# Kernel tuning notes

Measured on AMD Instinct MI355X. Metric: run time of the kernel, lower is better.

The kernel has to match this reference:

```python
import jax, jax.numpy as jnp
import numpy as np

N_NODES = 50000
N_EDGES = 800000
N_GRAPHS = 256
IN_CH = 128
HID = 256
FFN = 256
OUT = 1


def xavier(key, shape):
    fan_in, fan_out = shape[0], shape[1]
    a = jnp.sqrt(6.0 / (fan_in + fan_out))
    return jax.random.uniform(key, shape, jnp.float32, -a, a)


def setup_inputs() -> dict:
    key = jax.random.key(0)
    ks = jax.random.split(key, 12)
    x = jax.random.normal(ks[0], (N_NODES, IN_CH), jnp.float32)
    edge_index = jax.random.randint(ks[1], (2, N_EDGES), 0, N_NODES, jnp.int32)
    batch = jnp.sort(jax.random.randint(ks[2], (N_NODES,), 0, N_GRAPHS, jnp.int32))
    return {
        "x": x,
        "edge_index": edge_index,
        "batch": batch,
        # GCNConv layers (glorot weight, zero bias as in PyG reset_parameters)
        "W1": xavier(ks[3], (IN_CH, HID)), "b1": jnp.zeros((HID,), jnp.float32),
        "W2": xavier(ks[4], (HID, HID)),   "b2": jnp.zeros((HID,), jnp.float32),
        "W3": xavier(ks[5], (HID, HID)),   "b3": jnp.zeros((HID,), jnp.float32),
        # FFN: Linear(HID, FFN) then final Linear(FFN, OUT)
        "Wf": xavier(ks[6], (HID, FFN)),   "bf": jnp.zeros((FFN,), jnp.float32),
        "Wo": xavier(ks[7], (FFN, OUT)),   "bo": jnp.zeros((OUT,), jnp.float32),
    }


def _gcn_norm(edge_index, n_nodes):
    # add self-loops, compute symmetric normalization D^-1/2 (A+I) D^-1/2
    loops = jnp.arange(n_nodes, dtype=edge_index.dtype)
    row = jnp.concatenate([edge_index[0], loops])
    col = jnp.concatenate([edge_index[1], loops])
    deg = jax.ops.segment_sum(jnp.ones_like(col, jnp.float32), col, num_segments=n_nodes)
    dis = jnp.where(deg > 0, jax.lax.rsqrt(jnp.maximum(deg, 1.0)), 0.0)
    norm = dis[row] * dis[col]  # [E+N]
    return row, col, norm


def _gcn_conv(x, W, b, row, col, norm, n_nodes):
    xw = x @ W                                   # [N, H]
    msg = xw[row] * norm[:, None]                # gather + scale  [E+N, H]
    out = jax.ops.segment_sum(msg, col, num_segments=n_nodes)
    return out + b


def reference(x, edge_index, batch, W1, b1, W2, b2, W3, b3, Wf, bf, Wo, bo):
    row, col, norm = _gcn_norm(edge_index, N_NODES)
    h = jax.nn.relu(_gcn_conv(x, W1, b1, row, col, norm, N_NODES))
    h = jax.nn.relu(_gcn_conv(h, W2, b2, row, col, norm, N_NODES))
    h = jax.nn.relu(_gcn_conv(h, W3, b3, row, col, norm, N_NODES))
    # global mean pool over graphs
    counts = jax.ops.segment_sum(jnp.ones((N_NODES,), jnp.float32), batch, num_segments=N_GRAPHS)
    pooled = jax.ops.segment_sum(h, batch, num_segments=N_GRAPHS) / jnp.maximum(counts, 1.0)[:, None]
    # FFN (dropout is identity in eval mode): Linear -> ReLU -> final Linear
    g = jax.nn.relu(pooled @ Wf + bf)
    out = g @ Wo + bo
    return out
```

## Files before the change

### kernel.cpp

```cpp
#include <hip/hip_runtime.h>
#include <hip/hip_bf16.h>
#include <hip/hip_fp16.h>


#define THREADS 256

typedef _Float16 f16x8 __attribute__((ext_vector_type(8)));
typedef float    f32x4 __attribute__((ext_vector_type(4)));
typedef unsigned short u16x8 __attribute__((ext_vector_type(8)));


__global__ void degree_goff_kernel(const int* __restrict__ col, int* __restrict__ deg, int E,
                                   const int* __restrict__ batch, int* __restrict__ goff,
                                   int N, int G) {
    int i = blockIdx.x * THREADS + threadIdx.x;
    if (i < E) atomicAdd(&deg[col[i]], 1);
    if (i < N) {
        int b1 = batch[i];
        int b0 = (i == 0) ? -1 : batch[i - 1];
        for (int g = b0 + 1; g <= b1; ++g) goff[g] = i;
        if (i == N - 1) {
            for (int g = b1 + 1; g <= G; ++g) goff[g] = N;
        }
    }
}

__global__ __launch_bounds__(256) void scanA_kernel(
    const int* __restrict__ in, int* __restrict__ out, int* __restrict__ bsum,
    float* __restrict__ dis, int n) {
    __shared__ int wsum[4];
    int i0 = blockIdx.x * 1024 + threadIdx.x * 4;
    int lane = threadIdx.x & 63, wid = threadIdx.x >> 6;
    int v0 = 0, v1 = 0, v2 = 0, v3 = 0;
    if (i0 + 3 < n) {
        int4 v = *(const int4*)&in[i0];
        v0 = v.x; v1 = v.y; v2 = v.z; v3 = v.w;
    } else {
        if (i0 + 0 < n) v0 = in[i0 + 0];
        if (i0 + 1 < n) v1 = in[i0 + 1];
        if (i0 + 2 < n) v2 = in[i0 + 2];
        if (i0 + 3 < n) v3 = in[i0 + 3];
    }
    if (i0 + 0 < n) dis[i0 + 0] = rsqrtf((float)(v0 + 1));
    if (i0 + 1 < n) dis[i0 + 1] = rsqrtf((float)(v1 + 1));
    if (i0 + 2 < n) dis[i0 + 2] = rsqrtf((float)(v2 + 1));
    if (i0 + 3 < n) dis[i0 + 3] = rsqrtf((float)(v3 + 1));
    v0 = (v0 + 7) & ~7; v1 = (v1 + 7) & ~7;
    v2 = (v2 + 7) & ~7; v3 = (v3 + 7) & ~7;
    int s = v0 + v1 + v2 + v3;
    int inc = s;
    #pragma unroll
    for (int d = 1; d < 64; d <<= 1) {
        int t = __shfl_up(inc, d);
        if (lane >= d) inc += t;
    }
    if (lane == 63) wsum[wid] = inc;
    __syncthreads();
    int add = 0;
    for (int w = 0; w < wid; ++w) add += wsum[w];
    int ex = add + inc - s;
    if (i0 + 0 < n) out[i0 + 0] = ex;
    if (i0 + 1 < n) out[i0 + 1] = ex + v0;
    if (i0 + 2 < n) out[i0 + 2] = ex + v0 + v1;
    if (i0 + 3 < n) out[i0 + 3] = ex + v0 + v1 + v2;
    if (threadIdx.x == 255) bsum[blockIdx.x] = add + inc;
}

__global__ void scanB_kernel(int* __restrict__ bsum, int* __restrict__ total_slot, int nb) {
    int lane = threadIdx.x;
    int v = (lane < nb) ? bsum[lane] : 0;
    int inc = v;
    #pragma unroll
    for (int d = 1; d < 64; d <<= 1) {
        int t = __shfl_up(inc, d);
        if (lane >= d) inc += t;
    }
    if (lane < nb) bsum[lane] = inc - v;
    if (lane == 63) *total_slot = inc;
}

__global__ void padfill_kernel(const int* __restrict__ offs, const int* __restrict__ deg,
                               unsigned short* __restrict__ srcs, int N) {
    int c = blockIdx.x * THREADS + threadIdx.x;
    if (c < N) {
        int s = offs[c] + deg[c], e = offs[c + 1];
        for (int i = s; i < e; ++i) srcs[i] = (unsigned short)N;
    }
}

__global__ void csr_fill_kernel(const int* __restrict__ row, const int* __restrict__ col,
                                const int* __restrict__ offs, int* __restrict__ deg,
                                unsigned short* __restrict__ srcs, int E) {
    int e = blockIdx.x * THREADS + threadIdx.x;
    if (e < E) {
        int c = col[e];
        int old = atomicSub(&deg[c], 1);
        srcs[offs[c] + old - 1] = (unsigned short)row[e];
    }
}

__global__ void convert_kernel(
    int* __restrict__ offs, const int* __restrict__ bsum, int Nfix,
    const float* __restrict__ X, const float* __restrict__ dis,
    _Float16* __restrict__ Xs, int total8, int IC,
    const float* __restrict__ W1, _Float16* __restrict__ W1t, int k1,
    const float* __restrict__ W2, _Float16* __restrict__ W2t,
    const float* __restrict__ W3, _Float16* __restrict__ W3t,
    _Float16* __restrict__ Hs) {
    int i = blockIdx.x * THREADS + threadIdx.x;
    if (i < Nfix) {
        offs[i] += bsum[i >> 10];
        return;
    }
    int j = i - Nfix;
    int Ms = Nfix + 1;
    if (j < total8) {
        int idx = j * 8;
        int node = idx / IC;
        int ch0  = idx % IC;
        float d = dis[node];
        float4 a = *(const float4*)&X[idx];
        float4 b = *(const float4*)&X[idx + 4];
        f16x8 o;
        o[0] = (_Float16)(d * a.x); o[1] = (_Float16)(d * a.y);
        o[2] = (_Float16)(d * a.z); o[3] = (_Float16)(d * a.w);
        o[4] = (_Float16)(d * b.x); o[5] = (_Float16)(d * b.y);
        o[6] = (_Float16)(d * b.z); o[7] = (_Float16)(d * b.w);
        int sw = IC >> 3;
        int slice = ch0 / sw, within = ch0 % sw;
        *(f16x8*)&Xs[((size_t)slice * Ms + node) * sw + within] = o;
        return;
    }
    j -= total8;
    int n1 = k1 * 256;
    if (j < n1) {
        int k = j >> 8, n = j & 255;
        W1t[n * k1 + k] = (_Float16)W1[j];
        return;
    }
    j -= n1;
    if (j < 65536) {
        int k = j >> 8, n = j & 255;
        W2t[n * 256 + k] = (_Float16)W2[j];
        return;
    }
    j -= 65536;
    if (j < 65536) {
        int k = j >> 8, n = j & 255;
        W3t[n * 256 + k] = (_Float16)W3[j];
        return;
    }
    j -= 65536;
    {
        int swx = IC >> 3;
        int nx = 8 * swx;
        if (j < nx) {
            int slice = j / swx, wi = j % swx;
            Xs[((size_t)slice * Ms + Nfix) * swx + wi] = (_Float16)0.f;
            return;
        }
        j -= nx;
        if (j < 256) {
            int slice = j >> 5, wi = j & 31;
            Hs[((size_t)slice * Ms + Nfix) * 32 + wi] = (_Float16)0.f;
        }
    }
}


template<int CH>
__global__ __launch_bounds__(256) void aggregate_slice_kernel(
    const _Float16* __restrict__ X, const int* __restrict__ offs,
    const unsigned short* __restrict__ srcs, const float* __restrict__ dis,
    _Float16* __restrict__ A, int N) {
    constexpr int LPN = CH / 64;
    constexpr int NPB = 256 / LPN;
    int bid   = blockIdx.x;
    int slice = bid & 7;
    int tile  = bid >> 3;
    int node  = tile * NPB + threadIdx.x / LPN;
    if (node >= N) return;
    int lane = threadIdx.x % LPN;
    size_t Ms = (size_t)N + 1;
    const f16x8* Xv = (const f16x8*)X + (size_t)slice * Ms * LPN;
    f16x8 self = Xv[(size_t)node * LPN + lane];
    float acc[8], acc2[8];
    #pragma unroll
    for (int j = 0; j < 8; ++j) { acc[j] = (float)self[j]; acc2[j] = 0.f; }
    int s = offs[node], e = offs[node + 1];
    int nit = (e - s) >> 3;
    if (nit > 0) {
        const u16x8* ip = (const u16x8*)&srcs[s];
        u16x8 idx = ip[0];
        for (int it = 0; it < nit; ++it) {
            u16x8 nxt = ip[min(it + 1, nit - 1)];
            f16x8 v0 = Xv[(size_t)idx[0] * LPN + lane];
            f16x8 v1 = Xv[(size_t)idx[1] * LPN + lane];
            f16x8 v2 = Xv[(size_t)idx[2] * LPN + lane];
            f16x8 v3 = Xv[(size_t)idx[3] * LPN + lane];
            f16x8 v4 = Xv[(size_t)idx[4] * LPN + lane];
            f16x8 v5 = Xv[(size_t)idx[5] * LPN + lane];
            f16x8 v6 = Xv[(size_t)idx[6] * LPN + lane];
            f16x8 v7 = Xv[(size_t)idx[7] * LPN + lane];
            #pragma unroll
            for (int j = 0; j < 8; ++j) {
                acc[j]  += ((float)v0[j] + (float)v2[j]) + ((float)v4[j] + (float)v6[j]);
                acc2[j] += ((float)v1[j] + (float)v3[j]) + ((float)v5[j] + (float)v7[j]);
            }
            idx = nxt;
        }
    }
    float dn = dis[node];
    f16x8 o;
    #pragma unroll
    for (int j = 0; j < 8; ++j) o[j] = (_Float16)(dn * (acc[j] + acc2[j]));
    f16x8* Av = (f16x8*)A + (size_t)slice * Ms * LPN;
    __builtin_nontemporal_store(o, &Av[(size_t)node * LPN + lane]);
}


template<int K, int MODE>
__global__ __launch_bounds__(256) void gemm_as_kernel(
    const _Float16* __restrict__ A, const _Float16* __restrict__ Bt,
    const float* __restrict__ bias, const float* __restrict__ dscale,
    _Float16* __restrict__ H, float* __restrict__ pooled,
    const int* __restrict__ batch, int M, int Ms) {
    constexpr int LSA = K + 40;
    constexpr int KC = K / 32;
    constexpr int SPR = K / 8;
    constexpr int SPS = K / 64;
    constexpr int SW  = K / 8;
    __shared__ _Float16 As[64 * LSA];
    int tid = threadIdx.x;
    int m0 = blockIdx.x * 64;

    {
        constexpr int RPI = 256 / SPR;
        int r_in = tid % RPI;
        int seg  = tid / RPI;
        int slice = seg / SPS, sub = seg % SPS;
        #pragma unroll
        for (int it = 0; it < 64 / RPI; ++it) {
            int r = it * RPI + r_in;
            int gr = m0 + r;
            uint4 v = make_uint4(0, 0, 0, 0);
            if (gr < M) v = *(const uint4*)&A[((size_t)slice * Ms + gr) * SW + sub * 8];
            *(uint4*)&As[r * LSA + seg * 8] = v;
        }
    }
    __syncthreads();

    int wid = tid >> 6, lane = tid & 63;
    int l16 = lane & 15, quad = lane >> 4;
    int wn = wid * 64;

    f32x4 acc[4][4] = {};
    const _Float16* Bbase = Bt + (size_t)(wn + l16) * K + quad * 8;

    #pragma unroll
    for (int kc = 0; kc < KC; ++kc) {
        f16x8 bh[4];
        #pragma unroll
        for (int ni = 0; ni < 4; ++ni)
            bh[ni] = *(const f16x8*)&Bbase[(size_t)(ni * 16) * K + kc * 32];
        #pragma unroll
        for (int mi = 0; mi < 4; ++mi) {
            f16x8 ah = *(const f16x8*)&As[(mi * 16 + l16) * LSA + kc * 32 + quad * 8];
            #pragma unroll
            for (int ni = 0; ni < 4; ++ni)
                acc[mi][ni] = __builtin_amdgcn_mfma_f32_16x16x32_f16(ah, bh[ni], acc[mi][ni], 0, 0, 0);
        }
    }

    #pragma unroll
    for (int mi = 0; mi < 4; ++mi) {
        int rbase = m0 + mi * 16;
        int g0 = 0, g15 = 0;
        if (MODE == 2) {
            g0  = batch[min(rbase, M - 1)];
            g15 = batch[min(rbase + 15, M - 1)];
        }
        #pragma unroll
        for (int ni = 0; ni < 4; ++ni) {
            int col = wn + ni * 16 + l16;
            float bv = bias[col];
            if (MODE == 1) {
                size_t hbase = (size_t)(col >> 5) * Ms * 32 + (col & 31);
                #pragma unroll
                for (int r = 0; r < 4; ++r) {
                    int grow = rbase + quad * 4 + r;
                    if (grow < M) {
                        float v = fmaxf(acc[mi][ni][r] + bv, 0.f) * dscale[grow];
                        H[hbase + (size_t)grow * 32] = (_Float16)v;
                    }
                }
            } else {
                if (g0 == g15) {
                    float p = 0.f;
                    #pragma unroll
                    for (int r = 0; r < 4; ++r) {
                        int grow = rbase + quad * 4 + r;
                        float v = fmaxf(acc[mi][ni][r] + bv, 0.f);
                        p += (grow < M) ? v : 0.f;
                    }
                    p += __shfl_xor(p, 16);
                    p += __shfl_xor(p, 32);
                    if (quad == 0) atomicAdd(&pooled[g0 * 256 + col], p);
                } else {
                    #pragma unroll
                    for (int r = 0; r < 4; ++r) {
                        int grow = rbase + quad * 4 + r;
                        if (grow < M) {
                            float v = fmaxf(acc[mi][ni][r] + bv, 0.f);
                            atomicAdd(&pooled[batch[grow] * 256 + col], v);
                        }
                    }
                }
            }
        }
    }
}


__global__ __launch_bounds__(256) void ffn_kernel(
    const float* __restrict__ pooled, const int* __restrict__ goff,
    const float* __restrict__ Wf, const float* __restrict__ bf,
    const float* __restrict__ Wo, const float* __restrict__ bo,
    float* __restrict__ out) {
    __shared__ float p[256];
    __shared__ float red[256];
    int g = blockIdx.x, t = threadIdx.x;
    int cnt = goff[g + 1] - goff[g];
    float inv = 1.f / (float)max(cnt, 1);
    p[t] = pooled[g * 256 + t] * inv;
    __syncthreads();
    float s = bf[t];
    #pragma unroll 8
    for (int k = 0; k < 256; ++k) s = fmaf(p[k], Wf[k * 256 + t], s);
    float gv = fmaxf(s, 0.f);
    red[t] = gv * Wo[t];
    __syncthreads();
    for (int o = 128; o > 0; o >>= 1) {
        if (t < o) red[t] += red[t + o];
        __syncthreads();
    }
    if (t == 0) out[g] = red[0] + bo[0];
}


extern "C" void kernel_launch(void* const* d_in, const int* in_sizes, int n_in,
                              void* d_out, int out_size, void* d_ws, size_t ws_size,
                              hipStream_t stream) {
    const float* x   = (const float*)d_in[0];
    const int*   ei  = (const int*)d_in[1];
    const int*   bat = (const int*)d_in[2];
    const float* W1  = (const float*)d_in[3];
    const float* b1  = (const float*)d_in[4];
    const float* W2  = (const float*)d_in[5];
    const float* b2  = (const float*)d_in[6];
    const float* W3  = (const float*)d_in[7];
    const float* b3  = (const float*)d_in[8];
    const float* Wf  = (const float*)d_in[9];
    const float* bf  = (const float*)d_in[10];
    const float* Wo  = (const float*)d_in[11];
    const float* bo  = (const float*)d_in[12];
    float* out = (float*)d_out;

    const int N  = in_sizes[2];
    const int E  = in_sizes[1] / 2;
    const int IC = in_sizes[0] / N;
    const int HID = 256;
    const int G  = out_size;
    const int Ms = N + 1;
    const int* row = ei;
    const int* col = ei + E;

    char* w = (char*)d_ws;
    size_t off = 0;
    auto alloc = [&](size_t bytes) -> void* {
        void* p = w + off;
        off += (bytes + 255) & ~(size_t)255;
        return p;
    };
    int*   deg    = (int*)alloc((size_t)N * 4);
    float* pooled = (float*)alloc((size_t)G * HID * 4);
    float* dis    = (float*)alloc((size_t)N * 4);
    int*   offs   = (int*)alloc((size_t)(N + 1) * 4);
    unsigned short* srcs = (unsigned short*)alloc(((size_t)E + 7 * (size_t)N + 8) * 2);
    int*   goff   = (int*)alloc((size_t)(G + 1) * 4);
    int*   bsum   = (int*)alloc((size_t)64 * 4);
    _Float16* W1t = (_Float16*)alloc((size_t)HID * IC * 2);
    _Float16* W2t = (_Float16*)alloc((size_t)HID * HID * 2);
    _Float16* W3t = (_Float16*)alloc((size_t)HID * HID * 2);
    _Float16* Xs  = (_Float16*)alloc((size_t)Ms * IC * 2);
    _Float16* Ah  = (_Float16*)alloc((size_t)Ms * HID * 2);
    _Float16* Hs  = (_Float16*)alloc((size_t)Ms * HID * 2);
    (void)ws_size; (void)n_in;

    size_t zlen = (((size_t)N * 4 + 255) & ~(size_t)255) + (size_t)G * HID * 4;
    hipMemsetAsync(deg, 0, zlen, stream);

    int nb = (N + 1023) / 1024;
    degree_goff_kernel<<<(E + THREADS - 1) / THREADS, THREADS, 0, stream>>>(
        col, deg, E, bat, goff, N, G);
    scanA_kernel<<<nb, 256, 0, stream>>>(deg, offs, bsum, dis, N);
    scanB_kernel<<<1, 64, 0, stream>>>(bsum, &offs[N], nb);

    int total8 = N * IC / 8;
    int conv_total = N + total8 + IC * HID + HID * HID + HID * HID + 8 * (IC / 8) + 256;
    convert_kernel<<<(conv_total + THREADS - 1) / THREADS, THREADS, 0, stream>>>(
        offs, bsum, N, x, dis, Xs, total8, IC, W1, W1t, IC, W2, W2t, W3, W3t, Hs);

    padfill_kernel<<<(N + THREADS - 1) / THREADS, THREADS, 0, stream>>>(offs, deg, srcs, N);
    csr_fill_kernel<<<(E + THREADS - 1) / THREADS, THREADS, 0, stream>>>(row, col, offs, deg, srcs, E);

    int mtiles = (N + 63) / 64;
    int nt1 = (N + 127) / 128;
    aggregate_slice_kernel<128><<<nt1 * 8, 256, 0, stream>>>(Xs, offs, srcs, dis, Ah, N);
    gemm_as_kernel<128, 1><<<mtiles, 256, 0, stream>>>(Ah, W1t, b1, dis, Hs, nullptr, nullptr, N, Ms);
    int nt2 = (N + 63) / 64;
    aggregate_slice_kernel<256><<<nt2 * 8, 256, 0, stream>>>(Hs, offs, srcs, dis, Ah, N);
    gemm_as_kernel<256, 1><<<mtiles, 256, 0, stream>>>(Ah, W2t, b2, dis, Hs, nullptr, nullptr, N, Ms);
    aggregate_slice_kernel<256><<<nt2 * 8, 256, 0, stream>>>(Hs, offs, srcs, dis, Ah, N);
    gemm_as_kernel<256, 2><<<mtiles, 256, 0, stream>>>(Ah, W3t, b3, nullptr, nullptr, pooled, bat, N, Ms);

    ffn_kernel<<<G, 256, 0, stream>>>(pooled, goff, Wf, bf, Wo, bo, out);
}
```

Measured before the change: 396.5 us.

## Partition CSR fill by destination-node slice across XCD-interleaved blocks

```diff
diff --git a/kernel.cpp b/kernel.cpp
--- a/kernel.cpp
+++ b/kernel.cpp
@@ -4,6 +4,7 @@
 
 
 #define THREADS 256
+#define EPB 2048
 
 typedef _Float16 f16x8 __attribute__((ext_vector_type(8)));
 typedef float    f32x4 __attribute__((ext_vector_type(4)));
@@ -79,23 +80,51 @@
     if (lane == 63) *total_slot = inc;
 }
 
-__global__ void padfill_kernel(const int* __restrict__ offs, const int* __restrict__ deg,
-                               unsigned short* __restrict__ srcs, int N) {
-    int c = blockIdx.x * THREADS + threadIdx.x;
-    if (c < N) {
-        int s = offs[c] + deg[c], e = offs[c + 1];
-        for (int i = s; i < e; ++i) srcs[i] = (unsigned short)N;
-    }
-}
-
-__global__ void csr_fill_kernel(const int* __restrict__ row, const int* __restrict__ col,
-                                const int* __restrict__ offs, int* __restrict__ deg,
-                                unsigned short* __restrict__ srcs, int E) {
-    int e = blockIdx.x * THREADS + threadIdx.x;
-    if (e < E) {
-        int c = col[e];
-        int old = atomicSub(&deg[c], 1);
-        srcs[offs[c] + old - 1] = (unsigned short)row[e];
+__global__ __launch_bounds__(256) void padfill_x_kernel(
+    const int* __restrict__ offs, const int* __restrict__ deg,
+    unsigned short* __restrict__ srcs, int N) {
+    int slice = blockIdx.x & 7;
+    int SL = (N + 7) >> 3;
+    int node = slice * SL + (int)(blockIdx.x >> 3) * THREADS + threadIdx.x;
+    int nhi = min(N, slice * SL + SL);
+    if (node >= nhi) return;
+    int s = offs[node] + deg[node], e = offs[node + 1];
+    for (int i = s; i < e; ++i) srcs[i] = (unsigned short)N;
+}
+
+__global__ __launch_bounds__(256) void csr_fill_x_kernel(
+    const int* __restrict__ row, const int* __restrict__ col,
+    const int* __restrict__ offs, int* __restrict__ deg,
+    unsigned short* __restrict__ srcs, int E, int N) {
+    int slice = blockIdx.x & 7;
+    int SL = (N + 7) >> 3;
+    int nlo = slice * SL;
+    int nhi = min(N, nlo + SL);
+    int e0 = (int)(blockIdx.x >> 3) * EPB + threadIdx.x * 8;
+    if (e0 >= E) return;
+    if (e0 + 8 <= E) {
+        int4 c0 = *(const int4*)&col[e0];
+        int4 c1 = *(const int4*)&col[e0 + 4];
+        int4 r0 = *(const int4*)&row[e0];
+        int4 r1 = *(const int4*)&row[e0 + 4];
+        int cs[8] = {c0.x, c0.y, c0.z, c0.w, c1.x, c1.y, c1.z, c1.w};
+        int rs[8] = {r0.x, r0.y, r0.z, r0.w, r1.x, r1.y, r1.z, r1.w};
+        #pragma unroll
+        for (int j = 0; j < 8; ++j) {
+            int c = cs[j];
+            if (c >= nlo && c < nhi) {
+                int old = atomicSub(&deg[c], 1);
+                srcs[offs[c] + old - 1] = (unsigned short)rs[j];
+            }
+        }
+    } else {
+        for (int j = 0; j < 8 && e0 + j < E; ++j) {
+            int c = col[e0 + j];
+            if (c >= nlo && c < nhi) {
+                int old = atomicSub(&deg[c], 1);
+                srcs[offs[c] + old - 1] = (unsigned short)row[e0 + j];
+            }
+        }
     }
 }
 
@@ -411,8 +440,11 @@
     convert_kernel<<<(conv_total + THREADS - 1) / THREADS, THREADS, 0, stream>>>(
         offs, bsum, N, x, dis, Xs, total8, IC, W1, W1t, IC, W2, W2t, W3, W3t, Hs);
 
-    padfill_kernel<<<(N + THREADS - 1) / THREADS, THREADS, 0, stream>>>(offs, deg, srcs, N);
-    csr_fill_kernel<<<(E + THREADS - 1) / THREADS, THREADS, 0, stream>>>(row, col, offs, deg, srcs, E);
+    int SL = (N + 7) >> 3;
+    int pf_tiles = (SL + THREADS - 1) / THREADS;
+    padfill_x_kernel<<<pf_tiles * 8, THREADS, 0, stream>>>(offs, deg, srcs, N);
+    int cf_chunks = (E + EPB - 1) / EPB;
+    csr_fill_x_kernel<<<cf_chunks * 8, THREADS, 0, stream>>>(row, col, offs, deg, srcs, E, N);
 
     int mtiles = (N + 63) / 64;
     int nt1 = (N + 127) / 128;
```

Result: no change. 392.2 us (-1.1%).
